# Kernel optimization log

Hardware: AMD Instinct MI355X
Metric: run time of the kernel (lower is better)

Reference implementation:

```python
import jax, jax.numpy as jnp
import numpy as np

F6_E3M2_MAX = 28.0  # max representable e3m2 value
M_TOKENS, K_IN, N_OUT = 256, 4096, 4096


def _quantize_e3m2(w: np.ndarray) -> np.ndarray:
    """Round-to-nearest onto the FP6 e3m2 grid (bias=3, min normal 2^-2, subnormal step 2^-4)."""
    sign = np.sign(w)
    a = np.minimum(np.abs(w), F6_E3M2_MAX)
    e = np.clip(np.floor(np.log2(np.maximum(a, 1e-30))), -2.0, 4.0)
    step = np.exp2(e - 2.0)  # 2 mantissa bits -> 4 steps per octave; subnormal step = 2^-4
    q = np.round(a / step) * step
    return (sign * np.minimum(q, F6_E3M2_MAX)).astype(np.float32)


def setup_inputs() -> dict:
    key = jax.random.key(0)
    k_x, k_w, k_b = jax.random.split(key, 3)
    x = (jax.random.normal(k_x, (M_TOKENS, K_IN), dtype=jnp.float32)).astype(jnp.float16)
    w_fp32 = np.asarray(jax.random.normal(k_w, (N_OUT, K_IN), dtype=jnp.float32)) * 0.02
    # per-row scale as in to_scaled_tc_float6_e3m2
    amax = np.clip(np.abs(w_fp32).max(axis=1), 1e-12, None)
    scale = F6_E3M2_MAX / amax                       # quantization scale
    weight_fp6 = _quantize_e3m2(w_fp32 * scale[:, None])  # values on the e3m2 grid
    scales = jnp.asarray(1.0 / scale, dtype=jnp.float16)  # dequant scale (stored half)
    bias = (jax.random.normal(k_b, (N_OUT,), dtype=jnp.float32) * 0.01).astype(jnp.float16)
    return {
        "x": x,
        "weight_fp6": jnp.asarray(weight_fp6),
        "scales": scales,
        "bias": bias,
    }


def reference(x, weight_fp6, scales, bias):
    # Fused dequant + GEMM: W = weight_fp6 * row_scale; out = x @ W^T + bias
    in_features = weight_fp6.shape[1]
    x2d = x.reshape(-1, in_features).astype(jnp.float16)
    w_deq = weight_fp6 * scales.astype(jnp.float32)[:, None]  # [N, K] fp32
    out = jnp.einsum("mk,nk->mn", x2d.astype(jnp.float32), w_deq,
                     preferred_element_type=jnp.float32)       # fp32 accumulate (split-K sums in fp32)
    out = out.astype(jnp.float16) + bias
    return out.reshape(*x.shape[:-1], weight_fp6.shape[0]).astype(x.dtype)
```

## Files before the change

### kernel.cpp

```cpp
#include <hip/hip_runtime.h>
#include <hip/hip_fp16.h>


typedef __attribute__((ext_vector_type(8))) _Float16 half8;
typedef __attribute__((ext_vector_type(4))) _Float16 half4;
typedef __attribute__((ext_vector_type(2))) __fp16 fp16x2;
typedef __attribute__((ext_vector_type(4))) float f32x4;

constexpr int K = 4096, N = 4096, M = 256;
constexpr int BM = 128, BN = 128, BK = 32;
constexpr int SPL = 8;
constexpr int KSPL = K / SPL;
constexpr int NT = KSPL / BK;

__device__ __forceinline__ half4 cvt4(float4 f) {
    fp16x2 p0 = __builtin_amdgcn_cvt_pkrtz(f.x, f.y);
    fp16x2 p1 = __builtin_amdgcn_cvt_pkrtz(f.z, f.w);
    half4 h;
    h[0]=(_Float16)p0[0]; h[1]=(_Float16)p0[1];
    h[2]=(_Float16)p1[0]; h[3]=(_Float16)p1[1];
    return h;
}

__global__ __launch_bounds__(256, 2)
void gemm(const float* __restrict__ X,
          const float* __restrict__ W,
          _Float16* __restrict__ P)
{
    __shared__ __align__(16) _Float16 LA[2][BM * BK];
    __shared__ __align__(16) _Float16 LB[2][BN * BK];

    const int tid = (int)threadIdx.x;
    const int l   = tid & 63;
    const int wv  = tid >> 6;
    const int lc  = l & 15;
    const int lr  = l >> 4;
    const int wm  = (wv & 1) * 64;
    const int wn  = (wv >> 1) * 64;

    const int bid = (int)blockIdx.x;
    const int xcd = bid & 7;
    const int i   = bid >> 3;
    const int mb  = i & 1;
    const int sp  = (i >> 1) & 7;
    const int nbl = i >> 4;
    const int bm  = mb * BM;
    const int bn  = (xcd * 4 + nbl) * BN;
    const int kb  = sp * KSPL;

    const int srow = wv * 32 + (l >> 3);
    const int scol = (l & 7) * 4;
    const float* ax0 = X + (size_t)(bm + srow)      * K + kb + scol;
    const float* ax1 = X + (size_t)(bm + srow + 8)  * K + kb + scol;
    const float* ax2 = X + (size_t)(bm + srow + 16) * K + kb + scol;
    const float* ax3 = X + (size_t)(bm + srow + 24) * K + kb + scol;
    const float* wx0 = W + (size_t)(bn + srow)      * K + kb + scol;
    const float* wx1 = W + (size_t)(bn + srow + 8)  * K + kb + scol;
    const float* wx2 = W + (size_t)(bn + srow + 16) * K + kb + scol;
    const float* wx3 = W + (size_t)(bn + srow + 24) * K + kb + scol;
    const int wr0 = srow * BK + (l & 7) * 4;

    float4 s0a0, s0a1, s0a2, s0a3, s0w0, s0w1, s0w2, s0w3;
    float4 s1a0, s1a1, s1a2, s1a3, s1w0, s1w1, s1w2, s1w3;

#define GLOAD0(t) do { const size_t o = (size_t)(t) * BK;               \
        s0a0 = *(const float4*)(ax0 + o); s0a1 = *(const float4*)(ax1 + o); \
        s0a2 = *(const float4*)(ax2 + o); s0a3 = *(const float4*)(ax3 + o); \
        s0w0 = *(const float4*)(wx0 + o); s0w1 = *(const float4*)(wx1 + o); \
        s0w2 = *(const float4*)(wx2 + o); s0w3 = *(const float4*)(wx3 + o); } while (0)
#define GLOAD1(t) do { const size_t o = (size_t)(t) * BK;               \
        s1a0 = *(const float4*)(ax0 + o); s1a1 = *(const float4*)(ax1 + o); \
        s1a2 = *(const float4*)(ax2 + o); s1a3 = *(const float4*)(ax3 + o); \
        s1w0 = *(const float4*)(wx0 + o); s1w1 = *(const float4*)(wx1 + o); \
        s1w2 = *(const float4*)(wx2 + o); s1w3 = *(const float4*)(wx3 + o); } while (0)
#define CVTW0(bf) do {                                                  \
        *(half4*)(&LA[bf][wr0])          = cvt4(s0a0);                  \
        *(half4*)(&LA[bf][wr0 + 8*BK])   = cvt4(s0a1);                  \
        *(half4*)(&LA[bf][wr0 + 16*BK])  = cvt4(s0a2);                  \
        *(half4*)(&LA[bf][wr0 + 24*BK])  = cvt4(s0a3);                  \
        *(half4*)(&LB[bf][wr0])          = cvt4(s0w0);                  \
        *(half4*)(&LB[bf][wr0 + 8*BK])   = cvt4(s0w1);                  \
        *(half4*)(&LB[bf][wr0 + 16*BK])  = cvt4(s0w2);                  \
        *(half4*)(&LB[bf][wr0 + 24*BK])  = cvt4(s0w3); } while (0)
#define CVTW1(bf) do {                                                  \
        *(half4*)(&LA[bf][wr0])          = cvt4(s1a0);                  \
        *(half4*)(&LA[bf][wr0 + 8*BK])   = cvt4(s1a1);                  \
        *(half4*)(&LA[bf][wr0 + 16*BK])  = cvt4(s1a2);                  \
        *(half4*)(&LA[bf][wr0 + 24*BK])  = cvt4(s1a3);                  \
        *(half4*)(&LB[bf][wr0])          = cvt4(s1w0);                  \
        *(half4*)(&LB[bf][wr0 + 8*BK])   = cvt4(s1w1);                  \
        *(half4*)(&LB[bf][wr0 + 16*BK])  = cvt4(s1w2);                  \
        *(half4*)(&LB[bf][wr0 + 24*BK])  = cvt4(s1w3); } while (0)

    f32x4 acc[4][4];
    #pragma unroll
    for (int a = 0; a < 4; ++a)
        #pragma unroll
        for (int b = 0; b < 4; ++b)
            acc[a][b] = (f32x4){0.f, 0.f, 0.f, 0.f};

#define COMPUTE(bf) do {                                                \
        half8 af[4], wf[4];                                             \
        _Pragma("unroll")                                               \
        for (int ar = 0; ar < 4; ++ar)                                  \
            af[ar] = *(const half8*)(&LA[bf][(wm + ar * 16 + lc) * BK + lr * 8]); \
        _Pragma("unroll")                                               \
        for (int br = 0; br < 4; ++br)                                  \
            wf[br] = *(const half8*)(&LB[bf][(wn + br * 16 + lc) * BK + lr * 8]); \
        _Pragma("unroll")                                               \
        for (int ar = 0; ar < 4; ++ar)                                  \
            _Pragma("unroll")                                           \
            for (int br = 0; br < 4; ++br)                              \
                acc[ar][br] = __builtin_amdgcn_mfma_f32_16x16x32_f16(   \
                    af[ar], wf[br], acc[ar][br], 0, 0, 0); } while (0)

    GLOAD0(0);
    GLOAD1(1);
    asm volatile("s_waitcnt vmcnt(8)" ::: "memory");
    CVTW0(0);
    asm volatile("s_waitcnt lgkmcnt(0)" ::: "memory");
    __builtin_amdgcn_s_barrier();

    for (int t = 0; t < NT; ++t) {
        const int tn = (t + 2 < NT) ? t + 2 : NT - 1;
        if (t & 1) GLOAD1(tn); else GLOAD0(tn);
        __builtin_amdgcn_sched_barrier(0);
        COMPUTE(t & 1);
        asm volatile("s_waitcnt vmcnt(8)" ::: "memory");
        __builtin_amdgcn_sched_barrier(0);
        if (t & 1) CVTW0((t + 1) & 1); else CVTW1((t + 1) & 1);
        asm volatile("s_waitcnt lgkmcnt(0)" ::: "memory");
        __builtin_amdgcn_s_barrier();
    }
#undef GLOAD0
#undef GLOAD1
#undef CVTW0
#undef CVTW1
#undef COMPUTE

    _Float16* Pb = P + (size_t)sp * M * N;
    const int orow = bm + wm + lr * 4;
    const int ocol = bn + wn + lc;
    #pragma unroll
    for (int ar = 0; ar < 4; ++ar)
        #pragma unroll
        for (int br = 0; br < 4; ++br)
            #pragma unroll
            for (int r = 0; r < 4; ++r)
                Pb[(size_t)(orow + ar * 16 + r) * N + ocol + br * 16]
                    = (_Float16)acc[ar][br][r];
}

__global__ __launch_bounds__(256)
void finalize(const _Float16* __restrict__ P,
              const float* __restrict__ S,
              const float* __restrict__ Bi,
              float* __restrict__ O)
{
    const size_t i = ((size_t)blockIdx.x * 256 + threadIdx.x) * 8;
    const int n = (int)(i & (N - 1));
    float acc[8] = {0.f, 0.f, 0.f, 0.f, 0.f, 0.f, 0.f, 0.f};
    #pragma unroll
    for (int s = 0; s < SPL; ++s) {
        half8 u = *(const half8*)(P + (size_t)s * M * N + i);
        #pragma unroll
        for (int e = 0; e < 8; ++e) acc[e] += (float)u[e];
    }
    float4 sc0 = *(const float4*)(S + n);
    float4 sc1 = *(const float4*)(S + n + 4);
    float4 bb0 = *(const float4*)(Bi + n);
    float4 bb1 = *(const float4*)(Bi + n + 4);
    float sc[8] = {sc0.x, sc0.y, sc0.z, sc0.w, sc1.x, sc1.y, sc1.z, sc1.w};
    float bb[8] = {bb0.x, bb0.y, bb0.z, bb0.w, bb1.x, bb1.y, bb1.z, bb1.w};
    float out[8];
    #pragma unroll
    for (int e = 0; e < 8; ++e)
        out[e] = (float)(_Float16)((float)(_Float16)(acc[e] * sc[e]) + bb[e]);
    *(float4*)(O + i)     = (float4){out[0], out[1], out[2], out[3]};
    *(float4*)(O + i + 4) = (float4){out[4], out[5], out[6], out[7]};
}

__global__ __launch_bounds__(256)
void fp6lin_small(const float* __restrict__ X, const float* __restrict__ W,
                  const float* __restrict__ S, const float* __restrict__ Bi,
                  float* __restrict__ O)
{
    const int n = (int)blockIdx.x;
    const int m = (int)threadIdx.x;
    float s = 0.f;
    for (int k = 0; k < K; ++k)
        s += (float)(_Float16)X[(size_t)m * K + k] * (float)(_Float16)W[(size_t)n * K + k];
    O[(size_t)m * N + n] = (float)(_Float16)((float)(_Float16)(s * S[n]) + Bi[n]);
}

extern "C" void kernel_launch(void* const* d_in, const int* in_sizes, int n_in,
                              void* d_out, int out_size, void* d_ws, size_t ws_size,
                              hipStream_t stream) {
    const float* x  = (const float*)d_in[0];
    const float* w  = (const float*)d_in[1];
    const float* s  = (const float*)d_in[2];
    const float* bi = (const float*)d_in[3];
    float* o = (float*)d_out;

    const size_t pbytes = (size_t)SPL * M * N * 2;
    _Float16* P = (_Float16*)d_ws;

    if (ws_size >= pbytes) {
        gemm<<<dim3(512), dim3(256), 0, stream>>>(x, w, P);
        finalize<<<dim3(M * N / 8 / 256), dim3(256), 0, stream>>>(P, s, bi, o);
    } else {
        fp6lin_small<<<dim3(N), dim3(M), 0, stream>>>(x, w, s, bi, o);
    }
}
```

Measured before the change: 33.17 us.

## Halve GEMM N-tile, double grid, and simplify prefetch to one stage

```diff
diff --git a/kernel.cpp b/kernel.cpp
--- a/kernel.cpp
+++ b/kernel.cpp
@@ -8,7 +8,7 @@
 typedef __attribute__((ext_vector_type(4))) float f32x4;
 
 constexpr int K = 4096, N = 4096, M = 256;
-constexpr int BM = 128, BN = 128, BK = 32;
+constexpr int BM = 128, BN = 64, BK = 32;
 constexpr int SPL = 8;
 constexpr int KSPL = K / SPL;
 constexpr int NT = KSPL / BK;
@@ -22,7 +22,7 @@
     return h;
 }
 
-__global__ __launch_bounds__(256, 2)
+__global__ __launch_bounds__(256, 4)
 void gemm(const float* __restrict__ X,
           const float* __restrict__ W,
           _Float16* __restrict__ P)
@@ -36,7 +36,7 @@
     const int lc  = l & 15;
     const int lr  = l >> 4;
     const int wm  = (wv & 1) * 64;
-    const int wn  = (wv >> 1) * 64;
+    const int wn  = (wv >> 1) * 32;
 
     const int bid = (int)blockIdx.x;
     const int xcd = bid & 7;
@@ -45,97 +45,79 @@
     const int sp  = (i >> 1) & 7;
     const int nbl = i >> 4;
     const int bm  = mb * BM;
-    const int bn  = (xcd * 4 + nbl) * BN;
+    const int bn  = (xcd * 8 + nbl) * BN;
     const int kb  = sp * KSPL;
 
-    const int srow = wv * 32 + (l >> 3);
+    const int arow = wv * 32 + (l >> 3);
+    const int wrow = wv * 16 + (l >> 3);
     const int scol = (l & 7) * 4;
-    const float* ax0 = X + (size_t)(bm + srow)      * K + kb + scol;
-    const float* ax1 = X + (size_t)(bm + srow + 8)  * K + kb + scol;
-    const float* ax2 = X + (size_t)(bm + srow + 16) * K + kb + scol;
-    const float* ax3 = X + (size_t)(bm + srow + 24) * K + kb + scol;
-    const float* wx0 = W + (size_t)(bn + srow)      * K + kb + scol;
-    const float* wx1 = W + (size_t)(bn + srow + 8)  * K + kb + scol;
-    const float* wx2 = W + (size_t)(bn + srow + 16) * K + kb + scol;
-    const float* wx3 = W + (size_t)(bn + srow + 24) * K + kb + scol;
-    const int wr0 = srow * BK + (l & 7) * 4;
+    const float* ax0 = X + (size_t)(bm + arow)      * K + kb + scol;
+    const float* ax1 = X + (size_t)(bm + arow + 8)  * K + kb + scol;
+    const float* ax2 = X + (size_t)(bm + arow + 16) * K + kb + scol;
+    const float* ax3 = X + (size_t)(bm + arow + 24) * K + kb + scol;
+    const float* wx0 = W + (size_t)(bn + wrow)      * K + kb + scol;
+    const float* wx1 = W + (size_t)(bn + wrow + 8)  * K + kb + scol;
+    const int awr = arow * BK + (l & 7) * 4;
+    const int wwr = wrow * BK + (l & 7) * 4;
 
-    float4 s0a0, s0a1, s0a2, s0a3, s0w0, s0w1, s0w2, s0w3;
-    float4 s1a0, s1a1, s1a2, s1a3, s1w0, s1w1, s1w2, s1w3;
+    float4 sa0, sa1, sa2, sa3, sw0, sw1;
 
-#define GLOAD0(t) do { const size_t o = (size_t)(t) * BK;               \
-        s0a0 = *(const float4*)(ax0 + o); s0a1 = *(const float4*)(ax1 + o); \
-        s0a2 = *(const float4*)(ax2 + o); s0a3 = *(const float4*)(ax3 + o); \
-        s0w0 = *(const float4*)(wx0 + o); s0w1 = *(const float4*)(wx1 + o); \
-        s0w2 = *(const float4*)(wx2 + o); s0w3 = *(const float4*)(wx3 + o); } while (0)
-#define GLOAD1(t) do { const size_t o = (size_t)(t) * BK;               \
-        s1a0 = *(const float4*)(ax0 + o); s1a1 = *(const float4*)(ax1 + o); \
-        s1a2 = *(const float4*)(ax2 + o); s1a3 = *(const float4*)(ax3 + o); \
-        s1w0 = *(const float4*)(wx0 + o); s1w1 = *(const float4*)(wx1 + o); \
-        s1w2 = *(const float4*)(wx2 + o); s1w3 = *(const float4*)(wx3 + o); } while (0)
-#define CVTW0(bf) do {                                                  \
-        *(half4*)(&LA[bf][wr0])          = cvt4(s0a0);                  \
-        *(half4*)(&LA[bf][wr0 + 8*BK])   = cvt4(s0a1);                  \
-        *(half4*)(&LA[bf][wr0 + 16*BK])  = cvt4(s0a2);                  \
-        *(half4*)(&LA[bf][wr0 + 24*BK])  = cvt4(s0a3);                  \
-        *(half4*)(&LB[bf][wr0])          = cvt4(s0w0);                  \
-        *(half4*)(&LB[bf][wr0 + 8*BK])   = cvt4(s0w1);                  \
-        *(half4*)(&LB[bf][wr0 + 16*BK])  = cvt4(s0w2);                  \
-        *(half4*)(&LB[bf][wr0 + 24*BK])  = cvt4(s0w3); } while (0)
-#define CVTW1(bf) do {                                                  \
-        *(half4*)(&LA[bf][wr0])          = cvt4(s1a0);                  \
-        *(half4*)(&LA[bf][wr0 + 8*BK])   = cvt4(s1a1);                  \
-        *(half4*)(&LA[bf][wr0 + 16*BK])  = cvt4(s1a2);                  \
-        *(half4*)(&LA[bf][wr0 + 24*BK])  = cvt4(s1a3);                  \
-        *(half4*)(&LB[bf][wr0])          = cvt4(s1w0);                  \
-        *(half4*)(&LB[bf][wr0 + 8*BK])   = cvt4(s1w1);                  \
-        *(half4*)(&LB[bf][wr0 + 16*BK])  = cvt4(s1w2);                  \
-        *(half4*)(&LB[bf][wr0 + 24*BK])  = cvt4(s1w3); } while (0)
+#define GLOAD(t) do { const size_t o = (size_t)(t) * BK;                \
+        sa0 = *(const float4*)(ax0 + o); sa1 = *(const float4*)(ax1 + o); \
+        sa2 = *(const float4*)(ax2 + o); sa3 = *(const float4*)(ax3 + o); \
+        sw0 = *(const float4*)(wx0 + o); sw1 = *(const float4*)(wx1 + o); } while (0)
+#define CVTW(bf) do {                                                   \
+        *(half4*)(&LA[bf][awr])         = cvt4(sa0);                    \
+        *(half4*)(&LA[bf][awr + 8*BK])  = cvt4(sa1);                    \
+        *(half4*)(&LA[bf][awr + 16*BK]) = cvt4(sa2);                    \
+        *(half4*)(&LA[bf][awr + 24*BK]) = cvt4(sa3);                    \
+        *(half4*)(&LB[bf][wwr])         = cvt4(sw0);                    \
+        *(half4*)(&LB[bf][wwr + 8*BK])  = cvt4(sw1); } while (0)
 
-    f32x4 acc[4][4];
+    f32x4 acc[4][2];
     #pragma unroll
     for (int a = 0; a < 4; ++a)
         #pragma unroll
-        for (int b = 0; b < 4; ++b)
+        for (int b = 0; b < 2; ++b)
             acc[a][b] = (f32x4){0.f, 0.f, 0.f, 0.f};
 
 #define COMPUTE(bf) do {                                                \
-        half8 af[4], wf[4];                                             \
+        half8 af[4], wf[2];                                             \
         _Pragma("unroll")                                               \
         for (int ar = 0; ar < 4; ++ar)                                  \
             af[ar] = *(const half8*)(&LA[bf][(wm + ar * 16 + lc) * BK + lr * 8]); \
         _Pragma("unroll")                                               \
-        for (int br = 0; br < 4; ++br)                                  \
+        for (int br = 0; br < 2; ++br)                                  \
             wf[br] = *(const half8*)(&LB[bf][(wn + br * 16 + lc) * BK + lr * 8]); \
         _Pragma("unroll")                                               \
         for (int ar = 0; ar < 4; ++ar)                                  \
             _Pragma("unroll")                                           \
-            for (int br = 0; br < 4; ++br)                              \
+            for (int br = 0; br < 2; ++br)                              \
                 acc[ar][br] = __builtin_amdgcn_mfma_f32_16x16x32_f16(   \
                     af[ar], wf[br], acc[ar][br], 0, 0, 0); } while (0)
 
-    GLOAD0(0);
-    GLOAD1(1);
-    asm volatile("s_waitcnt vmcnt(8)" ::: "memory");
-    CVTW0(0);
+    GLOAD(0);
+    asm volatile("s_waitcnt vmcnt(0)" ::: "memory");
+    CVTW(0);
     asm volatile("s_waitcnt lgkmcnt(0)" ::: "memory");
     __builtin_amdgcn_s_barrier();
 
     for (int t = 0; t < NT; ++t) {
-        const int tn = (t + 2 < NT) ? t + 2 : NT - 1;
-        if (t & 1) GLOAD1(tn); else GLOAD0(tn);
-        __builtin_amdgcn_sched_barrier(0);
+        if (t + 1 < NT) {
+            GLOAD(t + 1);
+            __builtin_amdgcn_sched_barrier(0);
+        }
         COMPUTE(t & 1);
-        asm volatile("s_waitcnt vmcnt(8)" ::: "memory");
-        __builtin_amdgcn_sched_barrier(0);
-        if (t & 1) CVTW0((t + 1) & 1); else CVTW1((t + 1) & 1);
-        asm volatile("s_waitcnt lgkmcnt(0)" ::: "memory");
-        __builtin_amdgcn_s_barrier();
+        if (t + 1 < NT) {
+            asm volatile("s_waitcnt vmcnt(0)" ::: "memory");
+            __builtin_amdgcn_sched_barrier(0);
+            CVTW((t + 1) & 1);
+            asm volatile("s_waitcnt lgkmcnt(0)" ::: "memory");
+            __builtin_amdgcn_s_barrier();
+        }
     }
-#undef GLOAD0
-#undef GLOAD1
-#undef CVTW0
-#undef CVTW1
+#undef GLOAD
+#undef CVTW
 #undef COMPUTE
 
     _Float16* Pb = P + (size_t)sp * M * N;
@@ -144,7 +126,7 @@
     #pragma unroll
     for (int ar = 0; ar < 4; ++ar)
         #pragma unroll
-        for (int br = 0; br < 4; ++br)
+        for (int br = 0; br < 2; ++br)
             #pragma unroll
             for (int r = 0; r < 4; ++r)
                 Pb[(size_t)(orow + ar * 16 + r) * N + ocol + br * 16]
@@ -206,7 +188,7 @@
     _Float16* P = (_Float16*)d_ws;
 
     if (ws_size >= pbytes) {
-        gemm<<<dim3(512), dim3(256), 0, stream>>>(x, w, P);
+        gemm<<<dim3(1024), dim3(256), 0, stream>>>(x, w, P);
         finalize<<<dim3(M * N / 8 / 256), dim3(256), 0, stream>>>(P, s, bi, o);
     } else {
         fp6lin_small<<<dim3(N), dim3(M), 0, stream>>>(x, w, s, bi, o);
```

New measurement: 30.61 us, median of 2. 1.08x faster.
